# Kernel tuning notes

Measured on AMD Instinct MI355X. Metric: run time of the kernel, lower is better.

## Reference

```python
import jax, jax.numpy as jnp
import numpy as np

N, K, C = 32768, 64, 256
PAIR, HID, BINS, CLIP = 32, 64, 16, 32
LN_EPS = 1e-5


def setup_inputs() -> dict:
    key = jax.random.key(0)
    ks = jax.random.split(key, 12)
    inp = {
        "features": jax.random.normal(ks[0], (N, C), jnp.float32),
        "resi": jnp.arange(N, dtype=jnp.int32),
        "chain": jax.random.randint(ks[1], (N,), 0, 4, jnp.int32),
        "batch": jax.random.randint(ks[2], (N,), 0, 8, jnp.int32),
        "neighbours": jax.random.randint(ks[3], (N, K), 0, N, jnp.int32),
        # learned params
        "W_left": jax.random.normal(ks[4], (C, PAIR), jnp.float32) / np.sqrt(C),
        "W_right": jax.random.normal(ks[5], (C, PAIR), jnp.float32) / np.sqrt(C),
        "W_pos": jax.random.normal(ks[6], (2 * CLIP + 1, PAIR), jnp.float32) * 0.1,
        "ln_scale": jnp.ones((PAIR,), jnp.float32),
        "ln_bias": jnp.zeros((PAIR,), jnp.float32),
        "W1": jax.random.normal(ks[7], (PAIR, HID), jnp.float32) / np.sqrt(PAIR),
        "b1": jnp.zeros((HID,), jnp.float32),
        "W2": jax.random.normal(ks[8], (HID, BINS), jnp.float32) / np.sqrt(HID),
        "b2": jnp.zeros((BINS,), jnp.float32),
    }
    return inp


def reference(features, resi, chain, batch, neighbours,
              W_left, W_right, W_pos, ln_scale, ln_bias, W1, b1, W2, b2):
    # left/right 32-dim codes, pairwise combine via neighbour gather: [N,K,32]
    left = features @ W_left
    right = features @ W_right
    dcode = left[:, None, :] + right[neighbours]

    # relative sequence position one-hot (65 classes) -> Linear(32, bias=False).
    # one_hot @ W_pos == row-gather of W_pos; masked to same chain & batch.
    rel = jnp.clip(resi[neighbours] - resi[:, None], -CLIP, CLIP) + CLIP  # [N,K]
    same = (chain[neighbours] == chain[:, None]) & (batch[neighbours] == batch[:, None])
    dcode = dcode + jnp.where(same[..., None], W_pos[rel], 0.0)

    # LayerNorm over last axis (scale + offset)
    mu = dcode.mean(-1, keepdims=True)
    var = jnp.mean(jnp.square(dcode - mu), -1, keepdims=True)
    dcode = (dcode - mu) * jax.lax.rsqrt(var + LN_EPS) * ln_scale + ln_bias

    # 2-layer GELU MLP -> 16 bins
    h = jax.nn.gelu(dcode @ W1 + b1)
    logits = h @ W2 + b2
    log_p = jax.nn.log_softmax(logits, axis=-1)

    # softmax-weighted expected distance over bin centers of [0, 22) A
    step = 22.0 / BINS
    bin_centers = (jnp.arange(BINS, dtype=jnp.float32) + 0.5) * step
    dmap = (jnp.exp(log_p) * bin_centers).sum(axis=-1)  # [N,K]
    return log_p, dmap
```

## Files before the change

### kernel.cpp

```cpp
#include <hip/hip_runtime.h>
#include <stdint.h>

#define N_RES 32768
#define KNEI  64
#define CFEAT 256
#define PAIRD 32
#define HIDD  64
#define NBINS 16
#define CLIPV 32
#define NGROUPS (N_RES * KNEI / 16)

typedef __attribute__((ext_vector_type(8))) short  short8;
typedef __attribute__((ext_vector_type(4))) float  float4_t;

union U8 { uint32_t u[4]; short8 s8; };

__device__ __forceinline__ uint32_t pkbf(float a, float b) {
    uint32_t ua = __float_as_uint(a) + 0x8000u;
    uint32_t ub = __float_as_uint(b) + 0x8000u;
    uint32_t d;
    const uint32_t sel = 0x07060302u;
    asm("v_perm_b32 %0, %1, %2, %3" : "=v"(d) : "v"(ub), "v"(ua), "s"(sel));
    return d;
}
__device__ __forceinline__ float bflo(uint32_t w) { return __uint_as_float(w << 16); }
__device__ __forceinline__ float bfhi(uint32_t w) { return __uint_as_float(w & 0xFFFF0000u); }

__device__ __forceinline__ float fastrcp(float x) { return __builtin_amdgcn_rcpf(x); }
__device__ __forceinline__ float fexp2(float x)   { return __builtin_amdgcn_exp2f(x); }
__device__ __forceinline__ float flog2(float x)   { return __builtin_amdgcn_logf(x); }

__device__ __forceinline__ float gelu_tanh(float x) {
    const float k1 = 2.3022082f;
    const float k2 = 0.1029432f;
    float x2 = x * x;
    float t  = __builtin_fmaf(k2, x2, k1);
    float e  = fexp2(x * t);
    float th = __builtin_fmaf(-2.0f, fastrcp(e + 1.0f), 1.0f);
    float hx = 0.5f * x;
    return __builtin_fmaf(hx, th, hx);
}

__global__ __launch_bounds__(256) void proj_kernel(
    const float* __restrict__ feat, const float* __restrict__ Wl,
    const float* __restrict__ Wr, const int* __restrict__ resi,
    const int* __restrict__ chain, const int* __restrict__ batch,
    const float* __restrict__ wpos,
    uint4* __restrict__ leftbf, uint4* __restrict__ rightbf,
    uint32_t* __restrict__ meta, uint32_t* __restrict__ wposbf)
{
    __shared__ __align__(16) float Wc[CFEAT * 64];
    const int tid = threadIdx.x;
    for (int idx = tid; idx < CFEAT * 32; idx += 256) {
        int k = idx >> 5, o = idx & 31;
        Wc[k * 64 + o]      = Wl[idx];
        Wc[k * 64 + 32 + o] = Wr[idx];
    }
    const int row_base = blockIdx.x * 64;
    if (tid < 64) {
        int r = row_base + tid;
        meta[r] = (uint32_t)resi[r] | ((uint32_t)chain[r] << 16)
                | ((uint32_t)batch[r] << 19);
    }
    if (blockIdx.x == 0) {
        for (int i = tid; i < (2 * CLIPV + 1) * PAIRD / 2; i += 256)
            wposbf[i] = pkbf(wpos[2 * i], wpos[2 * i + 1]);
    }
    __syncthreads();

    const int cb = (tid & 7) * 8;
    const int r0 = row_base + (tid >> 3) * 2;

    float acc[2][8];
#pragma unroll
    for (int r = 0; r < 2; ++r)
#pragma unroll
        for (int j = 0; j < 8; ++j) acc[r][j] = 0.f;

    for (int i = 0; i < CFEAT; i += 4) {
        float4_t f0 = *(const float4_t*)(feat + (size_t)r0 * CFEAT + i);
        float4_t f1 = *(const float4_t*)(feat + (size_t)(r0 + 1) * CFEAT + i);
#pragma unroll
        for (int s = 0; s < 4; ++s) {
            float4_t wa = *(const float4_t*)(Wc + (i + s) * 64 + cb);
            float4_t wb = *(const float4_t*)(Wc + (i + s) * 64 + cb + 4);
#pragma unroll
            for (int j = 0; j < 4; ++j) {
                acc[0][j]     += f0[s] * wa[j];
                acc[0][4 + j] += f0[s] * wb[j];
                acc[1][j]     += f1[s] * wa[j];
                acc[1][4 + j] += f1[s] * wb[j];
            }
        }
    }
#pragma unroll
    for (int r = 0; r < 2; ++r) {
        uint4 o;
        o.x = pkbf(acc[r][0], acc[r][1]);
        o.y = pkbf(acc[r][2], acc[r][3]);
        o.z = pkbf(acc[r][4], acc[r][5]);
        o.w = pkbf(acc[r][6], acc[r][7]);
        if (cb < 32) leftbf [(size_t)(r0 + r) * 4 + (cb >> 3)]        = o;
        else         rightbf[(size_t)(r0 + r) * 4 + ((cb - 32) >> 3)] = o;
    }
}

__global__ __launch_bounds__(256, 8) void pair_kernel(
    const uint4* __restrict__ leftbf, const uint4* __restrict__ rightbf,
    const uint32_t* __restrict__ meta, const int* __restrict__ nbr,
    const uint32_t* __restrict__ wposbf,
    const float* __restrict__ lnS, const float* __restrict__ lnB,
    const float* __restrict__ W1, const float* __restrict__ b1,
    const float* __restrict__ W2, const float* __restrict__ b2,
    float* __restrict__ out_logp, float* __restrict__ out_dmap)
{
    __shared__ __align__(16) unsigned char Hbuf[4][16 * 144];
    __shared__ __align__(16) float b1p[HIDD];

    const int tid    = threadIdx.x;
    const int lane   = tid & 63;
    const int wlocal = tid >> 6;
    const int q      = lane >> 4;
    const int c      = lane & 15;

    if (tid < HIDD) {
        float s = b1[tid];
        for (int k = 0; k < PAIRD; ++k)
            s = __builtin_fmaf(lnB[k], W1[k * HIDD + tid], s);
        b1p[tid] = s;
    }

    short8 w1a[4];
#pragma unroll
    for (int t = 0; t < 4; ++t) {
        U8 tmp;
#pragma unroll
        for (int v = 0; v < 4; ++v) {
            int k0 = q * 8 + 2 * v, k1 = k0 + 1;
            float a0 = lnS[k0] * W1[k0 * HIDD + 16 * t + c];
            float a1 = lnS[k1] * W1[k1 * HIDD + 16 * t + c];
            tmp.u[v] = pkbf(a0, a1);
        }
        w1a[t] = tmp.s8;
    }
    short8 w2a[2];
#pragma unroll
    for (int kt = 0; kt < 2; ++kt) {
        U8 tmp;
#pragma unroll
        for (int v = 0; v < 4; ++v) {
            int k0 = kt * 32 + q * 8 + 2 * v;
            tmp.u[v] = pkbf(W2[k0 * NBINS + c], W2[(k0 + 1) * NBINS + c]);
        }
        w2a[kt] = tmp.s8;
    }
    const float4_t b2f = *(const float4_t*)(b2 + 4 * q);

    __syncthreads();

    const int wglobal = (blockIdx.x * 256 + tid) >> 6;
    const int stride  = 8192;

    uint4 lfS, rfS, pwS; float mskS;
    {
        const int pbase = wglobal * 16;
        const int n = pbase >> 6, p = pbase + c;
        const int nb = nbr[p];
        const uint32_t mn = meta[n];
        const uint32_t mb = meta[nb];
        lfS = leftbf [(size_t)n  * 4 + q];
        rfS = rightbf[(size_t)nb * 4 + q];
        int rel = min(max((int)(mb & 0xFFFFu) - (int)(mn & 0xFFFFu), -CLIPV), CLIPV) + CLIPV;
        mskS = (((mb ^ mn) & 0xFFFF0000u) == 0u) ? 1.0f : 0.0f;
        pwS = *(const uint4*)(wposbf + rel * 16 + q * 4);
    }

    for (int it = 0; it < 16; ++it) {
        const int gc = wglobal + it * stride;
        const int p  = gc * 16 + c;

        const int gn = wglobal + ((it + 1) & 15) * stride;
        const int nn = (gn * 16) >> 6, pn = gn * 16 + c;
        const int nbN = nbr[pn];
        const uint32_t mnN = meta[nn];
        const uint4 lfN = leftbf[(size_t)nn * 4 + q];

        const uint4 lf = lfS, rf = rfS, pw = pwS;
        const float msk = mskS;

        const uint32_t mbN = meta[nbN];
        const uint4 rfN = rightbf[(size_t)nbN * 4 + q];

        const uint32_t la[4] = {lf.x, lf.y, lf.z, lf.w};
        const uint32_t ra[4] = {rf.x, rf.y, rf.z, rf.w};
        const uint32_t pa[4] = {pw.x, pw.y, pw.z, pw.w};
        float d[8];
#pragma unroll
        for (int v = 0; v < 4; ++v) {
            d[2 * v]     = __builtin_fmaf(msk, bflo(pa[v]), bflo(la[v]) + bflo(ra[v]));
            d[2 * v + 1] = __builtin_fmaf(msk, bfhi(pa[v]), bfhi(la[v]) + bfhi(ra[v]));
        }

        float s1 = 0.f, s2 = 0.f;
#pragma unroll
        for (int j = 0; j < 8; ++j) { s1 += d[j]; s2 = __builtin_fmaf(d[j], d[j], s2); }
        s1 += __shfl_xor(s1, 16, 64);  s1 += __shfl_xor(s1, 32, 64);
        s2 += __shfl_xor(s2, 16, 64);  s2 += __shfl_xor(s2, 32, 64);
        const float mu   = s1 * (1.0f / 32.0f);
        const float var  = __builtin_fmaf(-mu, mu, s2 * (1.0f / 32.0f));
        const float rstd = __builtin_amdgcn_rsqf(var + 1e-5f);
        const float sh   = -mu * rstd;

        U8 dpack;
#pragma unroll
        for (int v = 0; v < 4; ++v) {
            float nA = __builtin_fmaf(d[2 * v],     rstd, sh);
            float nB = __builtin_fmaf(d[2 * v + 1], rstd, sh);
            dpack.u[v] = pkbf(nA, nB);
        }
        const short8 dfrag = dpack.s8;

        float4_t hacc[4];
#pragma unroll
        for (int t = 0; t < 4; ++t) {
            float4_t c1 = *(const float4_t*)(b1p + 16 * t + 4 * q);
            hacc[t] = __builtin_amdgcn_mfma_f32_16x16x32_bf16(w1a[t], dfrag, c1, 0, 0, 0);
        }

        const int relN = min(max((int)(mbN & 0xFFFFu) - (int)(mnN & 0xFFFFu),
                                 -CLIPV), CLIPV) + CLIPV;
        const float mskN = (((mbN ^ mnN) & 0xFFFF0000u) == 0u) ? 1.0f : 0.0f;
        const uint4 pwN = *(const uint4*)(wposbf + relN * 16 + q * 4);

        unsigned char* hb = &Hbuf[wlocal][0] + c * 144;
#pragma unroll
        for (int t = 0; t < 4; ++t) {
            float g0 = gelu_tanh(hacc[t][0]);
            float g1 = gelu_tanh(hacc[t][1]);
            float g2 = gelu_tanh(hacc[t][2]);
            float g3 = gelu_tanh(hacc[t][3]);
            uint2 w; w.x = pkbf(g0, g1); w.y = pkbf(g2, g3);
            *(uint2*)(hb + 32 * t + 8 * q) = w;
        }
        const short8 hf0 = *(const short8*)(hb + 16 * q);
        const short8 hf1 = *(const short8*)(hb + 64 + 16 * q);

        float4_t lacc;
        lacc = __builtin_amdgcn_mfma_f32_16x16x32_bf16(w2a[0], hf0, b2f,  0, 0, 0);
        lacc = __builtin_amdgcn_mfma_f32_16x16x32_bf16(w2a[1], hf1, lacc, 0, 0, 0);

        const float LOG2E = 1.4426950408889634f, LN2 = 0.6931471805599453f;
        float e[4];
#pragma unroll
        for (int r = 0; r < 4; ++r) e[r] = fexp2(lacc[r] * LOG2E);
        float ssum = (e[0] + e[1]) + (e[2] + e[3]);
        ssum += __shfl_xor(ssum, 16, 64);
        ssum += __shfl_xor(ssum, 32, 64);
        const float lse = flog2(ssum) * LN2;

        float4_t lp = {lacc[0] - lse, lacc[1] - lse, lacc[2] - lse, lacc[3] - lse};
        *(float4_t*)(out_logp + (size_t)p * NBINS + 4 * q) = lp;

        const float step  = 22.0f / NBINS;
        const float cbase = (4 * q + 0.5f) * step;
        float dpart = e[0] * cbase + e[1] * (cbase + step)
                    + e[2] * (cbase + 2 * step) + e[3] * (cbase + 3 * step);
        dpart += __shfl_xor(dpart, 16, 64);
        dpart += __shfl_xor(dpart, 32, 64);
        if (q == 0) out_dmap[p] = dpart * fastrcp(ssum);

        lfS = lfN; rfS = rfN; pwS = pwN; mskS = mskN;
    }
}

extern "C" void kernel_launch(void* const* d_in, const int* in_sizes, int n_in,
                              void* d_out, int out_size, void* d_ws, size_t ws_size,
                              hipStream_t stream) {
    const float* features = (const float*)d_in[0];
    const int*   resi     = (const int*)d_in[1];
    const int*   chain    = (const int*)d_in[2];
    const int*   batch    = (const int*)d_in[3];
    const int*   nbr      = (const int*)d_in[4];
    const float* W_left   = (const float*)d_in[5];
    const float* W_right  = (const float*)d_in[6];
    const float* W_pos    = (const float*)d_in[7];
    const float* ln_scale = (const float*)d_in[8];
    const float* ln_bias  = (const float*)d_in[9];
    const float* W1       = (const float*)d_in[10];
    const float* b1       = (const float*)d_in[11];
    const float* W2       = (const float*)d_in[12];
    const float* b2       = (const float*)d_in[13];

    char* ws = (char*)d_ws;
    uint4*    leftbf  = (uint4*)ws;
    uint4*    rightbf = (uint4*)(ws + (size_t)N_RES * 64);
    uint32_t* meta    = (uint32_t*)(ws + (size_t)2 * N_RES * 64);
    uint32_t* wposbf  = (uint32_t*)(ws + (size_t)2 * N_RES * 64 + N_RES * 4);

    float* out_logp = (float*)d_out;
    float* out_dmap = out_logp + (size_t)N_RES * KNEI * NBINS;

    proj_kernel<<<N_RES / 64, 256, 0, stream>>>(features, W_left, W_right,
                                                resi, chain, batch, W_pos,
                                                leftbf, rightbf, meta, wposbf);
    pair_kernel<<<2048, 256, 0, stream>>>(leftbf, rightbf, meta, nbr, wposbf,
                                          ln_scale, ln_bias, W1, b1, W2, b2,
                                          out_logp, out_dmap);
}
```

Measured before the change: 341.5 us.

## Split projection by half, drop software prefetch, use nontemporal output stores

The projection kernel now launches twice as many blocks, each computing either the left or the right projection with half the shared-memory weight tile, so more blocks can run at once. The pair kernel drops its manual next-iteration prefetch in favour of a plain grid-stride loop. It also loads neighbour indices and stores log-probs and distances with nontemporal hints to keep the streaming traffic out of the cache. Dropping the prefetch may expose gather latency, though the kernel's high occupancy may hide it, and the split doubles the feature-row reads in the projection.

```diff
diff --git a/kernel.cpp b/kernel.cpp
--- a/kernel.cpp
+++ b/kernel.cpp
@@ -49,16 +49,17 @@
     uint4* __restrict__ leftbf, uint4* __restrict__ rightbf,
     uint32_t* __restrict__ meta, uint32_t* __restrict__ wposbf)
 {
-    __shared__ __align__(16) float Wc[CFEAT * 64];
-    const int tid = threadIdx.x;
-    for (int idx = tid; idx < CFEAT * 32; idx += 256) {
-        int k = idx >> 5, o = idx & 31;
-        Wc[k * 64 + o]      = Wl[idx];
-        Wc[k * 64 + 32 + o] = Wr[idx];
-    }
-    const int row_base = blockIdx.x * 64;
-    if (tid < 64) {
-        int r = row_base + tid;
+    __shared__ __align__(16) float Wc[CFEAT * 32];
+    const int tid   = threadIdx.x;
+    const int half  = blockIdx.x >> 9;
+    const int rb    = (blockIdx.x & 511) * 64;
+    const float* W  = half ? Wr : Wl;
+    uint4* outtb    = half ? rightbf : leftbf;
+
+    for (int idx = tid; idx < CFEAT * 32; idx += 256)
+        Wc[idx] = W[idx];
+    if (half == 0 && tid < 64) {
+        int r = rb + tid;
         meta[r] = (uint32_t)resi[r] | ((uint32_t)chain[r] << 16)
                 | ((uint32_t)batch[r] << 19);
     }
@@ -68,41 +69,35 @@
     }
     __syncthreads();
 
-    const int cb = (tid & 7) * 8;
-    const int r0 = row_base + (tid >> 3) * 2;
-
-    float acc[2][8];
-#pragma unroll
-    for (int r = 0; r < 2; ++r)
-#pragma unroll
-        for (int j = 0; j < 8; ++j) acc[r][j] = 0.f;
+    const int cb  = (tid & 3) * 8;
+    const int row = rb + (tid >> 2);
+
+    float acc[8];
+#pragma unroll
+    for (int j = 0; j < 8; ++j) acc[j] = 0.f;
 
     for (int i = 0; i < CFEAT; i += 4) {
-        float4_t f0 = *(const float4_t*)(feat + (size_t)r0 * CFEAT + i);
-        float4_t f1 = *(const float4_t*)(feat + (size_t)(r0 + 1) * CFEAT + i);
+        float4_t f = *(const float4_t*)(feat + (size_t)row * CFEAT + i);
 #pragma unroll
         for (int s = 0; s < 4; ++s) {
-            float4_t wa = *(const float4_t*)(Wc + (i + s) * 64 + cb);
-            float4_t wb = *(const float4_t*)(Wc + (i + s) * 64 + cb + 4);
+            float4_t wa = *(const float4_t*)(Wc + (i + s) * 32 + cb);
+            float4_t wb = *(const float4_t*)(Wc + (i + s) * 32 + cb + 4);
 #pragma unroll
             for (int j = 0; j < 4; ++j) {
-                acc[0][j]     += f0[s] * wa[j];
-                acc[0][4 + j] += f0[s] * wb[j];
-                acc[1][j]     += f1[s] * wa[j];
-                acc[1][4 + j] += f1[s] * wb[j];
+                acc[j]     = __builtin_fmaf(f[s], wa[j], acc[j]);
+                acc[4 + j] = __builtin_fmaf(f[s], wb[j], acc[4 + j]);
             }
         }
     }
-#pragma unroll
-    for (int r = 0; r < 2; ++r) {
-        uint4 o;
-        o.x = pkbf(acc[r][0], acc[r][1]);
-        o.y = pkbf(acc[r][2], acc[r][3]);
-        o.z = pkbf(acc[r][4], acc[r][5]);
-        o.w = pkbf(acc[r][6], acc[r][7]);
-        if (cb < 32) leftbf [(size_t)(r0 + r) * 4 + (cb >> 3)]        = o;
-        else         rightbf[(size_t)(r0 + r) * 4 + ((cb - 32) >> 3)] = o;
-    }
+    uint2 o;
+    o.x = pkbf(acc[0], acc[1]);
+    o.y = pkbf(acc[2], acc[3]);
+    uint2 o2;
+    o2.x = pkbf(acc[4], acc[5]);
+    o2.y = pkbf(acc[6], acc[7]);
+    uint2* dst = (uint2*)outtb + (size_t)row * 8 + (cb >> 2);
+    dst[0] = o;
+    dst[1] = o2;
 }
 
 __global__ __launch_bounds__(256, 8) void pair_kernel(
@@ -159,37 +154,23 @@
     __syncthreads();
 
     const int wglobal = (blockIdx.x * 256 + tid) >> 6;
-    const int stride  = 8192;
-
-    uint4 lfS, rfS, pwS; float mskS;
-    {
-        const int pbase = wglobal * 16;
-        const int n = pbase >> 6, p = pbase + c;
-        const int nb = nbr[p];
+    const int nwaves  = (gridDim.x * 256) >> 6;
+
+    for (int g = wglobal; g < NGROUPS; g += nwaves) {
+        const int pbase = g * 16;
+        const int n = pbase >> 6;
+        const int p = pbase + c;
+        const int nb = __builtin_nontemporal_load(nbr + p);
+
         const uint32_t mn = meta[n];
         const uint32_t mb = meta[nb];
-        lfS = leftbf [(size_t)n  * 4 + q];
-        rfS = rightbf[(size_t)nb * 4 + q];
-        int rel = min(max((int)(mb & 0xFFFFu) - (int)(mn & 0xFFFFu), -CLIPV), CLIPV) + CLIPV;
-        mskS = (((mb ^ mn) & 0xFFFF0000u) == 0u) ? 1.0f : 0.0f;
-        pwS = *(const uint4*)(wposbf + rel * 16 + q * 4);
-    }
-
-    for (int it = 0; it < 16; ++it) {
-        const int gc = wglobal + it * stride;
-        const int p  = gc * 16 + c;
-
-        const int gn = wglobal + ((it + 1) & 15) * stride;
-        const int nn = (gn * 16) >> 6, pn = gn * 16 + c;
-        const int nbN = nbr[pn];
-        const uint32_t mnN = meta[nn];
-        const uint4 lfN = leftbf[(size_t)nn * 4 + q];
-
-        const uint4 lf = lfS, rf = rfS, pw = pwS;
-        const float msk = mskS;
-
-        const uint32_t mbN = meta[nbN];
-        const uint4 rfN = rightbf[(size_t)nbN * 4 + q];
+        const uint4 lf = leftbf [(size_t)n  * 4 + q];
+        const uint4 rf = rightbf[(size_t)nb * 4 + q];
+
+        const int rel = min(max((int)(mb & 0xFFFFu) - (int)(mn & 0xFFFFu),
+                                -CLIPV), CLIPV) + CLIPV;
+        const float msk = (((mb ^ mn) & 0xFFFF0000u) == 0u) ? 1.0f : 0.0f;
+        const uint4 pw = *(const uint4*)(wposbf + rel * 16 + q * 4);
 
         const uint32_t la[4] = {lf.x, lf.y, lf.z, lf.w};
         const uint32_t ra[4] = {rf.x, rf.y, rf.z, rf.w};
@@ -227,11 +208,6 @@
             hacc[t] = __builtin_amdgcn_mfma_f32_16x16x32_bf16(w1a[t], dfrag, c1, 0, 0, 0);
         }
 
-        const int relN = min(max((int)(mbN & 0xFFFFu) - (int)(mnN & 0xFFFFu),
-                                 -CLIPV), CLIPV) + CLIPV;
-        const float mskN = (((mbN ^ mnN) & 0xFFFF0000u) == 0u) ? 1.0f : 0.0f;
-        const uint4 pwN = *(const uint4*)(wposbf + relN * 16 + q * 4);
-
         unsigned char* hb = &Hbuf[wlocal][0] + c * 144;
 #pragma unroll
         for (int t = 0; t < 4; ++t) {
@@ -259,7 +235,7 @@
         const float lse = flog2(ssum) * LN2;
 
         float4_t lp = {lacc[0] - lse, lacc[1] - lse, lacc[2] - lse, lacc[3] - lse};
-        *(float4_t*)(out_logp + (size_t)p * NBINS + 4 * q) = lp;
+        __builtin_nontemporal_store(lp, (float4_t*)(out_logp + (size_t)p * NBINS + 4 * q));
 
         const float step  = 22.0f / NBINS;
         const float cbase = (4 * q + 0.5f) * step;
@@ -267,9 +243,8 @@
                     + e[2] * (cbase + 2 * step) + e[3] * (cbase + 3 * step);
         dpart += __shfl_xor(dpart, 16, 64);
         dpart += __shfl_xor(dpart, 32, 64);
-        if (q == 0) out_dmap[p] = dpart * fastrcp(ssum);
-
-        lfS = lfN; rfS = rfN; pwS = pwN; mskS = mskN;
+        if (q == 0)
+            __builtin_nontemporal_store(dpart * fastrcp(ssum), out_dmap + p);
     }
 }
 
@@ -300,9 +275,9 @@
     float* out_logp = (float*)d_out;
     float* out_dmap = out_logp + (size_t)N_RES * KNEI * NBINS;
 
-    proj_kernel<<<N_RES / 64, 256, 0, stream>>>(features, W_left, W_right,
-                                                resi, chain, batch, W_pos,
-                                                leftbf, rightbf, meta, wposbf);
+    proj_kernel<<<1024, 256, 0, stream>>>(features, W_left, W_right,
+                                          resi, chain, batch, W_pos,
+                                          leftbf, rightbf, meta, wposbf);
     pair_kernel<<<2048, 256, 0, stream>>>(leftbf, rightbf, meta, nbr, wposbf,
                                           ln_scale, ln_bias, W1, b1, W2, b2,
                                           out_logp, out_dmap);
```

Measured after the change: 290.2 us. 15.0% less time.
